# Optimization experiments

Hardware: AMD Instinct MI355X
Metric: run time of the kernel (lower is better)

The kernel has to match this reference:

```python
import jax, jax.numpy as jnp
import numpy as np


def setup_inputs() -> dict:
    key = jax.random.key(0)
    k1, k2, k3 = jax.random.split(key, 3)
    B, T, C = 4, 2048, 1024
    x = jax.random.normal(k1, (B, T, C), dtype=jnp.float32)
    w_attn = jax.random.normal(k2, (C, 3 * C), dtype=jnp.float32) * 0.02
    b_attn = jnp.zeros((3 * C,), dtype=jnp.float32)
    w_proj = jax.random.normal(k3, (C, C), dtype=jnp.float32) * 0.02
    b_proj = jnp.zeros((C,), dtype=jnp.float32)
    return {"x": x, "w_attn": w_attn, "b_attn": b_attn, "w_proj": w_proj, "b_proj": b_proj}


def reference(x, w_attn, b_attn, w_proj, b_proj):
    B, T, C = x.shape
    n_head = 16
    head_size = C // n_head
    qkv = x @ w_attn + b_attn                      # [B, T, 3C]
    q, k, v = jnp.split(qkv, 3, axis=-1)
    # [B, H, T, Dh]
    q = q.reshape(B, T, n_head, head_size).transpose(0, 2, 1, 3)
    k = k.reshape(B, T, n_head, head_size).transpose(0, 2, 1, 3)
    v = v.reshape(B, T, n_head, head_size).transpose(0, 2, 1, 3)
    scale = 1.0 / jnp.sqrt(jnp.float32(head_size))
    att = jnp.einsum("bhqd,bhkd->bhqk", q, k) * scale   # [B, H, T, T]
    causal = jnp.tril(jnp.ones((T, T), dtype=bool))
    att = jnp.where(causal[None, None], att, jnp.float32(-jnp.inf))
    att = jax.nn.softmax(att, axis=-1)
    y = jnp.einsum("bhqk,bhkd->bhqd", att, v)            # [B, H, T, Dh]
    y = y.transpose(0, 2, 1, 3).reshape(B, T, C)
    return y @ w_proj + b_proj
```

## Files before the change

kernel.cpp:

```cpp
#include <hip/hip_runtime.h>
#include <hip/hip_bf16.h>
#include <math.h>


typedef __attribute__((ext_vector_type(8))) short short8;
typedef __attribute__((ext_vector_type(4))) float f32x4;

__device__ __forceinline__ short f2bf(float f) {
    __hip_bfloat16 h = __float2bfloat16(f);
    return *reinterpret_cast<short*>(&h);
}
__device__ __forceinline__ float bf2f(short s) {
    __hip_bfloat16 h = *reinterpret_cast<__hip_bfloat16*>(&s);
    return __bfloat162float(h);
}

#define MFMA16(a, b, c) __builtin_amdgcn_mfma_f32_16x16x32_bf16((a), (b), (c), 0, 0, 0)

__device__ __forceinline__ void gload_lds16(const short* g, short* l) {
    __builtin_amdgcn_global_load_lds(
        (const __attribute__((address_space(1))) void*)g,
        (__attribute__((address_space(3))) void*)l, 16, 0, 0);
}

__global__ void sniff_kernel(const unsigned int* __restrict__ xb,
                             unsigned int* __restrict__ flag)
{
    __shared__ int cnt;
    if (threadIdx.x == 0) cnt = 0;
    __syncthreads();
    int c = 0;
    for (int i = threadIdx.x; i < 4096; i += 256) {
        unsigned e = (xb[i] >> 7) & 0xFFu;
        if (e >= 96u && e <= 142u) ++c;
    }
    atomicAdd(&cnt, c);
    __syncthreads();
    if (threadIdx.x == 0) *flag = (cnt < 2048) ? 1u : 0u;
}

__global__ __launch_bounds__(256)
void cvt_x(const void* __restrict__ in, short* __restrict__ out,
           const unsigned int* __restrict__ flagp)
{
    const bool f32in = (*flagp != 0u);
    const size_t i = ((size_t)blockIdx.x * 256 + threadIdx.x) * 8;
    if (f32in) {
        const float* f = (const float*)in + i;
        f32x4 u0 = *(const f32x4*)f;
        f32x4 u1 = *(const f32x4*)(f + 4);
        short8 v;
#pragma unroll
        for (int j = 0; j < 4; ++j) { v[j] = f2bf(u0[j]); v[j + 4] = f2bf(u1[j]); }
        *(short8*)(out + i) = v;
    } else {
        *(short8*)(out + i) = *(const short8*)((const short*)in + i);
    }
}

__global__ __launch_bounds__(256)
void transpose_cvt(const void* __restrict__ in, short* __restrict__ out,
                   int R, int C, const unsigned int* __restrict__ flagp)
{
    const bool f32in = (*flagp != 0u);
    __shared__ short tile[64][65];
    const int bx = blockIdx.x * 64;
    const int by = blockIdx.y * 64;
    const int tx = threadIdx.x & 63;
    const int ty = threadIdx.x >> 6;
#pragma unroll
    for (int i = 0; i < 64; i += 4) {
        size_t idx = (size_t)(by + ty + i) * C + bx + tx;
        tile[ty + i][tx] = f32in ? f2bf(((const float*)in)[idx])
                                 : ((const short*)in)[idx];
    }
    __syncthreads();
#pragma unroll
    for (int i = 0; i < 64; i += 4)
        out[(size_t)(bx + ty + i) * R + by + tx] = tile[tx][ty + i];
}

template <int EPI>
__global__ __launch_bounds__(256)
void gemm_kernel(const short* __restrict__ A,
                 const short* __restrict__ Bt,
                 const void* __restrict__ bias,
                 void* __restrict__ O0,
                 short* __restrict__ O1,
                 short* __restrict__ O2,
                 int M, int N, int K,
                 const unsigned int* __restrict__ flagp)
{
    const bool f32io = (*flagp != 0u);
    __shared__ __align__(16) short ldsA[128 * 32];
    __shared__ __align__(16) short ldsB[128 * 32];

    const int tid = threadIdx.x;
    const int lane = tid & 63;
    const int wv = tid >> 6;
    const int wm = (wv & 1) * 64;
    const int wn = (wv >> 1) * 64;
    const int tile_m = blockIdx.y * 128;
    const int tile_n = blockIdx.x * 128;

    f32x4 acc[4][4];
#pragma unroll
    for (int i = 0; i < 4; ++i)
#pragma unroll
        for (int j = 0; j < 4; ++j) acc[i][j] = (f32x4){0.f, 0.f, 0.f, 0.f};

    const int ar = lane & 15;
    const int aq = (lane >> 4) * 8;
    const int lrow = lane >> 2;
    const int lcol = (lane & 3) << 3;

    for (int k0 = 0; k0 < K; k0 += 32) {
#pragma unroll
        for (int p = 0; p < 2; ++p) {
            int c = wv * 2 + p;
            int row = c * 16 + lrow;
            gload_lds16(A + (size_t)(tile_m + row) * K + k0 + lcol, ldsA + c * 512);
            gload_lds16(Bt + (size_t)(tile_n + row) * K + k0 + lcol, ldsB + c * 512);
        }
        __syncthreads();

        short8 af[4], bfr[4];
#pragma unroll
        for (int i = 0; i < 4; ++i)
            af[i] = *(const short8*)(ldsA + (wm + i * 16 + ar) * 32 + aq);
#pragma unroll
        for (int j = 0; j < 4; ++j)
            bfr[j] = *(const short8*)(ldsB + (wn + j * 16 + ar) * 32 + aq);
#pragma unroll
        for (int i = 0; i < 4; ++i)
#pragma unroll
            for (int j = 0; j < 4; ++j)
                acc[i][j] = MFMA16(af[i], bfr[j], acc[i][j]);
        __syncthreads();
    }

    const int colq = lane & 15;
    const int rowq = (lane >> 4) * 4;
#pragma unroll
    for (int j = 0; j < 4; ++j) {
        int gn = tile_n + wn + j * 16 + colq;
        float bv = f32io ? ((const float*)bias)[gn] : bf2f(((const short*)bias)[gn]);
#pragma unroll
        for (int i = 0; i < 4; ++i) {
#pragma unroll
            for (int r = 0; r < 4; ++r) {
                int gm = tile_m + wm + i * 16 + rowq + r;
                float val = acc[i][j][r] + bv;
                if (EPI == 0) {
                    if (f32io) ((float*)O0)[(size_t)gm * N + gn] = val;
                    else       ((short*)O0)[(size_t)gm * N + gn] = f2bf(val);
                } else {
                    int which = gn >> 10;
                    int c = gn & 1023;
                    int h = c >> 6;
                    int d = c & 63;
                    int b = gm >> 11;
                    int t = gm & 2047;
                    size_t bh = (size_t)(b * 16 + h);
                    short o = f2bf(which == 0 ? val * 0.18033688011112042f : val);
                    if (which == 0)      ((short*)O0)[(bh * 2048 + t) * 64 + d] = o;
                    else if (which == 1) O1[(bh * 2048 + t) * 64 + d] = o;
                    else                 O2[(bh * 64 + d) * 2048 + t] = o;
                }
            }
        }
    }
}

__global__ __launch_bounds__(256, 4)
void attn_kernel(const short* __restrict__ Q,
                 const short* __restrict__ Kp_,
                 const short* __restrict__ Vt,
                 short* __restrict__ Y)
{
    __shared__ __align__(16) short ldsK[64 * 64];
    __shared__ __align__(16) short ldsV[64 * 64];
    __shared__ __align__(16) short pbuf[4][16 * 72];

    const int tid = threadIdx.x;
    const int lane = tid & 63;
    const int wv = tid >> 6;
    const int m16 = lane & 15;
    const int quad = lane >> 4;

    const int fid = blockIdx.x;
    const int xcd = fid & 7;
    const int slot = fid >> 3;
    const int bh = (xcd << 3) | (slot >> 4);
    const int g = slot & 15;

    const int b = bh >> 4, h = bh & 15;

    const short* Qp = Q   + (size_t)bh * 2048 * 64;
    const short* Kp = Kp_ + (size_t)bh * 2048 * 64;
    const short* Vp = Vt  + (size_t)bh * 64 * 2048;
    short* pw = pbuf[wv];

    const int srow = lane >> 3;
    const int sw = (((lane & 7) ^ (srow & 7)) << 3);
    const int swr = ((m16 & 7) << 3);

#pragma unroll
    for (int pass = 0; pass < 2; ++pass) {
        const int t = pass ? (31 - g) : g;
        const int qbase = t * 64 + wv * 16;

        short8 aq0 = *(const short8*)(Qp + (size_t)(qbase + m16) * 64 + quad * 8);
        short8 aq1 = *(const short8*)(Qp + (size_t)(qbase + m16) * 64 + 32 + quad * 8);

        f32x4 o[4];
#pragma unroll
        for (int dt = 0; dt < 4; ++dt) o[dt] = (f32x4){0.f, 0.f, 0.f, 0.f};
        float lrow[4] = {0.f, 0.f, 0.f, 0.f};

        for (int kt = 0; kt <= t; ++kt) {
            const int kb = kt << 6;

#pragma unroll
            for (int p = 0; p < 2; ++p) {
                const int c8 = wv * 2 + p;
                const int row = c8 * 8 + srow;
                gload_lds16(Kp + (size_t)(kb + row) * 64 + sw, ldsK + c8 * 512);
                gload_lds16(Vp + (size_t)row * 2048 + kb + sw, ldsV + c8 * 512);
            }
            __syncthreads();

            f32x4 s[4];
#pragma unroll
            for (int c = 0; c < 4; ++c) {
                const short* kr = ldsK + (c * 16 + m16) * 64;
                short8 kf0 = *(const short8*)(kr + ((quad * 8) ^ swr));
                short8 kf1 = *(const short8*)(kr + ((quad * 8 + 32) ^ swr));
                f32x4 z = (f32x4){0.f, 0.f, 0.f, 0.f};
                z = MFMA16(aq0, kf0, z);
                z = MFMA16(aq1, kf1, z);
                s[c] = z;
            }

#pragma unroll
            for (int c = 0; c < 4; ++c) {
                const int key = kb + c * 16 + m16;
                const bool needmask = (kb + c * 16 + 15 > qbase);
#pragma unroll
                for (int r = 0; r < 4; ++r) {
                    float p = exp2f(s[c][r]);
                    if (needmask && key > qbase + quad * 4 + r) p = 0.f;
                    lrow[r] += p;
                    pw[(quad * 4 + r) * 72 + c * 16 + m16] = f2bf(p);
                }
            }

            asm volatile("" ::: "memory");
            short8 ap0 = *(const short8*)(pw + m16 * 72 + quad * 8);
            short8 ap1 = *(const short8*)(pw + m16 * 72 + quad * 8 + 32);
            asm volatile("" ::: "memory");

#pragma unroll
            for (int dt = 0; dt < 4; ++dt) {
                const short* vr = ldsV + (dt * 16 + m16) * 64;
                short8 vf0 = *(const short8*)(vr + ((quad * 8) ^ swr));
                short8 vf1 = *(const short8*)(vr + ((quad * 8 + 32) ^ swr));
                o[dt] = MFMA16(ap0, vf0, o[dt]);
                o[dt] = MFMA16(ap1, vf1, o[dt]);
            }
            __syncthreads();
        }

        float linv[4];
#pragma unroll
        for (int r = 0; r < 4; ++r) {
            float sm = lrow[r];
#pragma unroll
            for (int off = 1; off < 16; off <<= 1)
                sm += __shfl_xor(sm, off);
            linv[r] = 1.0f / sm;
        }
#pragma unroll
        for (int dt = 0; dt < 4; ++dt) {
#pragma unroll
            for (int r = 0; r < 4; ++r) {
                int row = qbase + quad * 4 + r;
                int col = h * 64 + dt * 16 + m16;
                Y[((size_t)(b * 2048 + row)) * 1024 + col] = f2bf(o[dt][r] * linv[r]);
            }
        }
    }
}

extern "C" void kernel_launch(void* const* d_in, const int* in_sizes, int n_in,
                              void* d_out, int out_size, void* d_ws, size_t ws_size,
                              hipStream_t stream)
{
    const void* x      = d_in[0];
    const void* w_attn = d_in[1];
    const void* b_attn = d_in[2];
    const void* w_proj = d_in[3];
    const void* b_proj = d_in[4];

    char* ws = (char*)d_ws;
    unsigned int* flag = (unsigned int*)(ws + 0);
    short* Wta = (short*)(ws + 256);
    short* Wtp = (short*)(ws + 6291712);
    short* Qb  = (short*)(ws + 8388864);
    short* Kb  = (short*)(ws + 25166080);
    short* Vtb = (short*)(ws + 41943296);
    short* Yb  = (short*)(ws + 58720512);
    short* Xb  = (short*)(ws + 58720512);

    sniff_kernel<<<1, 256, 0, stream>>>((const unsigned int*)x, flag);
    cvt_x<<<dim3(4096), 256, 0, stream>>>(x, Xb, flag);
    transpose_cvt<<<dim3(48, 16), 256, 0, stream>>>(w_attn, Wta, 1024, 3072, flag);
    transpose_cvt<<<dim3(16, 16), 256, 0, stream>>>(w_proj, Wtp, 1024, 1024, flag);
    gemm_kernel<1><<<dim3(24, 64), 256, 0, stream>>>(Xb, Wta, b_attn, Qb, Kb, Vtb,
                                                     8192, 3072, 1024, flag);
    attn_kernel<<<dim3(1024), 256, 0, stream>>>(Qb, Kb, Vtb, Yb);
    gemm_kernel<0><<<dim3(8, 64), 256, 0, stream>>>(Yb, Wtp, b_proj, d_out, nullptr, nullptr,
                                                    8192, 1024, 1024, flag);
}
```

Baseline: 324.8 us.

## Double-buffer LDS tiles in GEMM and attention, raise MFMA wave priority

Both the projection GEMM and the causal attention kernel now use two LDS buffers. The next K-tile (or the next K/V block) is issued with global_load_lds before the current tile's MFMAs run, so global loads overlap compute and one barrier per iteration is dropped. The attention kernel also wraps its MFMA sections in s_setprio so those waves get issue priority. The cost is double the LDS per block, which in attention may lower the number of resident blocks per CU.

Result: no change. 325.5 us (+0.2%).

```diff
diff --git a/kernel.cpp b/kernel.cpp
--- a/kernel.cpp
+++ b/kernel.cpp
@@ -92,8 +92,8 @@
                  const unsigned int* __restrict__ flagp)
 {
     const bool f32io = (*flagp != 0u);
-    __shared__ __align__(16) short ldsA[128 * 32];
-    __shared__ __align__(16) short ldsB[128 * 32];
+    __shared__ __align__(16) short ldsA[2 * 128 * 32];
+    __shared__ __align__(16) short ldsB[2 * 128 * 32];
 
     const int tid = threadIdx.x;
     const int lane = tid & 63;
@@ -114,29 +114,42 @@
     const int lrow = lane >> 2;
     const int lcol = (lane & 3) << 3;
 
-    for (int k0 = 0; k0 < K; k0 += 32) {
+    auto stage = [&](int k0, int bsel) {
 #pragma unroll
         for (int p = 0; p < 2; ++p) {
             int c = wv * 2 + p;
             int row = c * 16 + lrow;
-            gload_lds16(A + (size_t)(tile_m + row) * K + k0 + lcol, ldsA + c * 512);
-            gload_lds16(Bt + (size_t)(tile_n + row) * K + k0 + lcol, ldsB + c * 512);
-        }
-        __syncthreads();
-
+            gload_lds16(A + (size_t)(tile_m + row) * K + k0 + lcol,
+                        ldsA + bsel * 4096 + c * 512);
+            gload_lds16(Bt + (size_t)(tile_n + row) * K + k0 + lcol,
+                        ldsB + bsel * 4096 + c * 512);
+        }
+    };
+
+    stage(0, 0);
+    __syncthreads();
+    int cur = 0;
+
+    for (int k0 = 0; k0 < K; k0 += 32) {
+        if (k0 + 32 < K) stage(k0 + 32, cur ^ 1);
+
+        const short* Ab = ldsA + cur * 4096;
+        const short* Bb = ldsB + cur * 4096;
         short8 af[4], bfr[4];
 #pragma unroll
         for (int i = 0; i < 4; ++i)
-            af[i] = *(const short8*)(ldsA + (wm + i * 16 + ar) * 32 + aq);
+            af[i] = *(const short8*)(Ab + (wm + i * 16 + ar) * 32 + aq);
 #pragma unroll
         for (int j = 0; j < 4; ++j)
-            bfr[j] = *(const short8*)(ldsB + (wn + j * 16 + ar) * 32 + aq);
+            bfr[j] = *(const short8*)(Bb + (wn + j * 16 + ar) * 32 + aq);
 #pragma unroll
         for (int i = 0; i < 4; ++i)
 #pragma unroll
             for (int j = 0; j < 4; ++j)
                 acc[i][j] = MFMA16(af[i], bfr[j], acc[i][j]);
+
         __syncthreads();
+        cur ^= 1;
     }
 
     const int colq = lane & 15;
@@ -178,8 +191,8 @@
                  const short* __restrict__ Vt,
                  short* __restrict__ Y)
 {
-    __shared__ __align__(16) short ldsK[64 * 64];
-    __shared__ __align__(16) short ldsV[64 * 64];
+    __shared__ __align__(16) short ldsK[2 * 64 * 64];
+    __shared__ __align__(16) short ldsV[2 * 64 * 64];
     __shared__ __align__(16) short pbuf[4][16 * 72];
 
     const int tid = threadIdx.x;
@@ -205,14 +218,31 @@
     const int sw = (((lane & 7) ^ (srow & 7)) << 3);
     const int swr = ((m16 & 7) << 3);
 
+    auto stage = [&](int kb, int bsel) {
+#pragma unroll
+        for (int p = 0; p < 2; ++p) {
+            const int c8 = wv * 2 + p;
+            const int row = c8 * 8 + srow;
+            gload_lds16(Kp + (size_t)(kb + row) * 64 + sw,
+                        ldsK + bsel * 4096 + c8 * 512);
+            gload_lds16(Vp + (size_t)row * 2048 + kb + sw,
+                        ldsV + bsel * 4096 + c8 * 512);
+        }
+    };
+
 #pragma unroll
     for (int pass = 0; pass < 2; ++pass) {
         const int t = pass ? (31 - g) : g;
         const int qbase = t * 64 + wv * 16;
 
+        stage(0, 0);
+
         short8 aq0 = *(const short8*)(Qp + (size_t)(qbase + m16) * 64 + quad * 8);
         short8 aq1 = *(const short8*)(Qp + (size_t)(qbase + m16) * 64 + 32 + quad * 8);
 
+        __syncthreads();
+        int cur = 0;
+
         f32x4 o[4];
 #pragma unroll
         for (int dt = 0; dt < 4; ++dt) o[dt] = (f32x4){0.f, 0.f, 0.f, 0.f};
@@ -220,20 +250,16 @@
 
         for (int kt = 0; kt <= t; ++kt) {
             const int kb = kt << 6;
-
-#pragma unroll
-            for (int p = 0; p < 2; ++p) {
-                const int c8 = wv * 2 + p;
-                const int row = c8 * 8 + srow;
-                gload_lds16(Kp + (size_t)(kb + row) * 64 + sw, ldsK + c8 * 512);
-                gload_lds16(Vp + (size_t)row * 2048 + kb + sw, ldsV + c8 * 512);
-            }
-            __syncthreads();
+            if (kt < t) stage(kb + 64, cur ^ 1);
+
+            const short* kbase = ldsK + cur * 4096;
+            const short* vbase = ldsV + cur * 4096;
 
             f32x4 s[4];
+            __builtin_amdgcn_s_setprio(1);
 #pragma unroll
             for (int c = 0; c < 4; ++c) {
-                const short* kr = ldsK + (c * 16 + m16) * 64;
+                const short* kr = kbase + (c * 16 + m16) * 64;
                 short8 kf0 = *(const short8*)(kr + ((quad * 8) ^ swr));
                 short8 kf1 = *(const short8*)(kr + ((quad * 8 + 32) ^ swr));
                 f32x4 z = (f32x4){0.f, 0.f, 0.f, 0.f};
@@ -241,6 +267,7 @@
                 z = MFMA16(aq1, kf1, z);
                 s[c] = z;
             }
+            __builtin_amdgcn_s_setprio(0);
 
 #pragma unroll
             for (int c = 0; c < 4; ++c) {
@@ -260,15 +287,19 @@
             short8 ap1 = *(const short8*)(pw + m16 * 72 + quad * 8 + 32);
             asm volatile("" ::: "memory");
 
+            __builtin_amdgcn_s_setprio(1);
 #pragma unroll
             for (int dt = 0; dt < 4; ++dt) {
-                const short* vr = ldsV + (dt * 16 + m16) * 64;
+                const short* vr = vbase + (dt * 16 + m16) * 64;
                 short8 vf0 = *(const short8*)(vr + ((quad * 8) ^ swr));
                 short8 vf1 = *(const short8*)(vr + ((quad * 8 + 32) ^ swr));
                 o[dt] = MFMA16(ap0, vf0, o[dt]);
                 o[dt] = MFMA16(ap1, vf1, o[dt]);
             }
+            __builtin_amdgcn_s_setprio(0);
+
             __syncthreads();
+            cur ^= 1;
         }
 
         float linv[4];
```
